# Kernel optimization log

Hardware: AMD Instinct MI355X
Metric: run time of the kernel (lower is better)

The kernel has to match this reference:

```python
import jax, jax.numpy as jnp
import numpy as np

KERNEL = 7
PAD = (KERNEL - 1) // 2


def setup_inputs() -> dict:
    key = jax.random.key(0)
    k1, k2 = jax.random.split(key)
    x = jax.random.normal(k1, (32, 256, 64, 64), dtype=jnp.float32)
    W = jax.random.normal(k2, (1, 2, KERNEL, KERNEL), dtype=jnp.float32) * 0.1
    return {"x": x, "W": W}


def reference(x, W):
    # channel-wise max and mean pooling -> [B, 2, H, W]
    x_compress = jnp.concatenate(
        [jnp.max(x, axis=1, keepdims=True), jnp.mean(x, axis=1, keepdims=True)],
        axis=1,
    )
    # 2->1 conv, same padding, no bias/bn/relu
    attn = jax.lax.conv_general_dilated(
        x_compress, W,
        window_strides=(1, 1),
        padding=[(PAD, PAD), (PAD, PAD)],
        dimension_numbers=("NCHW", "OIHW", "NCHW"),
    )
    scale = jax.nn.sigmoid(attn)  # [B, 1, H, W]
    return x * scale
```

## Files before the change

### kernel.cpp

```cpp
#include <hip/hip_runtime.h>
#include <math.h>

#define BB 32
#define CC 256
#define HH 64
#define WW 64
#define HWSZ 4096
#define CHW 1048576

typedef float f4 __attribute__((ext_vector_type(4)));

__global__ void sg_reduce(const float* __restrict__ x,
                          float* __restrict__ maxp,
                          float* __restrict__ meanp) {
    int bh = blockIdx.x;
    int b  = bh >> 6;
    int h  = bh & 63;
    int w4 = threadIdx.x & 15;
    int cg = threadIdx.x >> 4;

    const f4* base =
        reinterpret_cast<const f4*>(x + (size_t)b * CHW + h * WW) + w4;
    f4 v = base[(size_t)(cg * 16) * 1024];
    f4 mx = v, sm = v;
    #pragma unroll
    for (int cc = 1; cc < 16; ++cc) {
        f4 u = base[(size_t)(cg * 16 + cc) * 1024];
        mx.x = fmaxf(mx.x, u.x); mx.y = fmaxf(mx.y, u.y);
        mx.z = fmaxf(mx.z, u.z); mx.w = fmaxf(mx.w, u.w);
        sm += u;
    }

    __shared__ f4 lmax[16][16];
    __shared__ f4 lsum[16][16];
    lmax[cg][w4] = mx;
    lsum[cg][w4] = sm;
    __syncthreads();

    if (threadIdx.x < 16) {
        int w = threadIdx.x;
        f4 M = lmax[0][w];
        f4 S = lsum[0][w];
        #pragma unroll
        for (int g = 1; g < 16; ++g) {
            f4 m2 = lmax[g][w];
            S += lsum[g][w];
            M.x = fmaxf(M.x, m2.x); M.y = fmaxf(M.y, m2.y);
            M.z = fmaxf(M.z, m2.z); M.w = fmaxf(M.w, m2.w);
        }
        reinterpret_cast<f4*>(maxp)[bh * 16 + w] = M;
        reinterpret_cast<f4*>(meanp)[bh * 16 + w] = S * (1.0f / CC);
    }
}

__global__ void sg_conv_apply(const float* __restrict__ x,
                              const float* __restrict__ maxp,
                              const float* __restrict__ meanp,
                              const float* __restrict__ Wt,
                              float* __restrict__ out) {
    __shared__ float sscale[WW];
    int bh = blockIdx.x;
    int b  = bh >> 6;
    int h  = bh & 63;
    int tid = threadIdx.x;

    if (tid < WW) {
        int wc = tid;
        const float* mb = maxp  + b * HWSZ;
        const float* nb = meanp + b * HWSZ;
        float acc = 0.0f;
        #pragma unroll
        for (int kh = 0; kh < 7; ++kh) {
            int hh = h + kh - 3;
            if ((unsigned)hh >= (unsigned)HH) continue;
            #pragma unroll
            for (int kw = 0; kw < 7; ++kw) {
                int wcol = wc + kw - 3;
                if ((unsigned)wcol >= (unsigned)WW) continue;
                int o = (hh << 6) + wcol;
                acc = fmaf(mb[o], Wt[kh * 7 + kw],      acc);
                acc = fmaf(nb[o], Wt[49 + kh * 7 + kw], acc);
            }
        }
        sscale[wc] = 1.0f / (1.0f + __expf(-acc));
    }
    __syncthreads();

    int w4 = tid & 15;
    int cg = tid >> 4;
    f4 sc = reinterpret_cast<const f4*>(sscale)[w4];

    const f4* xb =
        reinterpret_cast<const f4*>(x + (size_t)b * CHW + h * WW) + w4;
    f4* ob =
        reinterpret_cast<f4*>(out + (size_t)b * CHW + h * WW) + w4;

    #pragma unroll
    for (int cc = 0; cc < 16; ++cc) {
        size_t off = (size_t)(cg * 16 + cc) * 1024;
        f4 v = xb[off];
        v *= sc;
        __builtin_nontemporal_store(v, ob + off);
    }
}

extern "C" void kernel_launch(void* const* d_in, const int* in_sizes, int n_in,
                              void* d_out, int out_size, void* d_ws, size_t ws_size,
                              hipStream_t stream) {
    const float* x  = (const float*)d_in[0];
    const float* Wt = (const float*)d_in[1];
    float* out = (float*)d_out;

    float* wsf   = (float*)d_ws;
    float* maxp  = wsf;
    float* meanp = wsf + BB * HWSZ;

    sg_reduce<<<BB * HH, 256, 0, stream>>>(x, maxp, meanp);
    sg_conv_apply<<<BB * HH, 256, 0, stream>>>(x, maxp, meanp, Wt, out);
}
```

Before: 73.10 us.

## Fuse reduce and conv-apply into one kernel with inter-block row flags

Merges the channel reduction and the conv/scale pass into a single kernel. Each block claims a row through an atomic ticket and keeps its 16 x-vectors per thread in registers, so x is read from HBM once instead of twice. It publishes its pooled row with a release flag and spins on flags for the neighbouring rows before computing the 7x7 conv. This adds a memset, spin-wait synchronisation and register pressure, and it relies on ticket ordering to avoid deadlock.

Result: slower. 276.7 us (+278.5%).

```diff
diff --git a/kernel.cpp b/kernel.cpp
--- a/kernel.cpp
+++ b/kernel.cpp
@@ -10,62 +10,84 @@
 
 typedef float f4 __attribute__((ext_vector_type(4)));
 
-__global__ void sg_reduce(const float* __restrict__ x,
-                          float* __restrict__ maxp,
-                          float* __restrict__ meanp) {
-    int bh = blockIdx.x;
-    int b  = bh >> 6;
-    int h  = bh & 63;
-    int w4 = threadIdx.x & 15;
-    int cg = threadIdx.x >> 4;
+__global__ void __launch_bounds__(256, 3)
+sg_fused(const float* __restrict__ x,
+         const float* __restrict__ Wt,
+         float* __restrict__ out,
+         float* __restrict__ maxp,
+         float* __restrict__ meanp,
+         int* __restrict__ flags,
+         int* __restrict__ ticket) {
+    __shared__ int s_row;
+    __shared__ float w_sh[98];
+    __shared__ alignas(16) float sscale[WW];
+    __shared__ f4 lmax[16][16];
+    __shared__ f4 lsum[16][16];
 
-    const f4* base =
+    int tid = threadIdx.x;
+    if (tid == 0) s_row = atomicAdd(ticket, 1);
+    if (tid < 98) w_sh[tid] = Wt[tid];
+    __syncthreads();
+
+    const int bh = s_row;
+    const int b  = bh >> 6;
+    const int h  = bh & 63;
+    const int w4 = tid & 15;
+    const int cg = tid >> 4;
+
+    const f4* xb =
         reinterpret_cast<const f4*>(x + (size_t)b * CHW + h * WW) + w4;
-    f4 v = base[(size_t)(cg * 16) * 1024];
-    f4 mx = v, sm = v;
+
+    f4 xr[16];
+    #pragma unroll
+    for (int cc = 0; cc < 16; ++cc)
+        xr[cc] = __builtin_nontemporal_load(xb + (size_t)(cg * 16 + cc) * 1024);
+
+    f4 mx = xr[0], sm = xr[0];
     #pragma unroll
     for (int cc = 1; cc < 16; ++cc) {
-        f4 u = base[(size_t)(cg * 16 + cc) * 1024];
+        f4 u = xr[cc];
         mx.x = fmaxf(mx.x, u.x); mx.y = fmaxf(mx.y, u.y);
         mx.z = fmaxf(mx.z, u.z); mx.w = fmaxf(mx.w, u.w);
         sm += u;
     }
-
-    __shared__ f4 lmax[16][16];
-    __shared__ f4 lsum[16][16];
     lmax[cg][w4] = mx;
     lsum[cg][w4] = sm;
     __syncthreads();
 
-    if (threadIdx.x < 16) {
-        int w = threadIdx.x;
-        f4 M = lmax[0][w];
-        f4 S = lsum[0][w];
+    if (tid < 16) {
+        f4 M = lmax[0][tid];
+        f4 S = lsum[0][tid];
         #pragma unroll
         for (int g = 1; g < 16; ++g) {
-            f4 m2 = lmax[g][w];
-            S += lsum[g][w];
+            f4 m2 = lmax[g][tid];
+            S += lsum[g][tid];
             M.x = fmaxf(M.x, m2.x); M.y = fmaxf(M.y, m2.y);
             M.z = fmaxf(M.z, m2.z); M.w = fmaxf(M.w, m2.w);
         }
-        reinterpret_cast<f4*>(maxp)[bh * 16 + w] = M;
-        reinterpret_cast<f4*>(meanp)[bh * 16 + w] = S * (1.0f / CC);
+        reinterpret_cast<f4*>(maxp)[bh * 16 + tid]  = M;
+        reinterpret_cast<f4*>(meanp)[bh * 16 + tid] = S * (1.0f / CC);
     }
-}
+    __syncthreads();
 
-__global__ void sg_conv_apply(const float* __restrict__ x,
-                              const float* __restrict__ maxp,
-                              const float* __restrict__ meanp,
-                              const float* __restrict__ Wt,
-                              float* __restrict__ out) {
-    __shared__ float sscale[WW];
-    int bh = blockIdx.x;
-    int b  = bh >> 6;
-    int h  = bh & 63;
-    int tid = threadIdx.x;
+    if (tid == 0) {
+        __threadfence();
+        __hip_atomic_store(&flags[bh], 1, __ATOMIC_RELEASE,
+                           __HIP_MEMORY_SCOPE_AGENT);
+    }
+    if (tid < 7) {
+        int hh = h - 3 + tid;
+        if (hh != h && (unsigned)hh < (unsigned)HH) {
+            const int dep = (b << 6) + hh;
+            while (__hip_atomic_load(&flags[dep], __ATOMIC_ACQUIRE,
+                                     __HIP_MEMORY_SCOPE_AGENT) == 0) {
+                __builtin_amdgcn_s_sleep(2);
+            }
+        }
+    }
+    __syncthreads();
 
     if (tid < WW) {
-        int wc = tid;
         const float* mb = maxp  + b * HWSZ;
         const float* nb = meanp + b * HWSZ;
         float acc = 0.0f;
@@ -75,32 +97,23 @@
             if ((unsigned)hh >= (unsigned)HH) continue;
             #pragma unroll
             for (int kw = 0; kw < 7; ++kw) {
-                int wcol = wc + kw - 3;
+                int wcol = tid + kw - 3;
                 if ((unsigned)wcol >= (unsigned)WW) continue;
                 int o = (hh << 6) + wcol;
-                acc = fmaf(mb[o], Wt[kh * 7 + kw],      acc);
-                acc = fmaf(nb[o], Wt[49 + kh * 7 + kw], acc);
+                acc = fmaf(mb[o], w_sh[kh * 7 + kw],      acc);
+                acc = fmaf(nb[o], w_sh[49 + kh * 7 + kw], acc);
             }
         }
-        sscale[wc] = 1.0f / (1.0f + __expf(-acc));
+        sscale[tid] = 1.0f / (1.0f + __expf(-acc));
     }
     __syncthreads();
 
-    int w4 = tid & 15;
-    int cg = tid >> 4;
     f4 sc = reinterpret_cast<const f4*>(sscale)[w4];
-
-    const f4* xb =
-        reinterpret_cast<const f4*>(x + (size_t)b * CHW + h * WW) + w4;
-    f4* ob =
-        reinterpret_cast<f4*>(out + (size_t)b * CHW + h * WW) + w4;
-
+    f4* ob = reinterpret_cast<f4*>(out + (size_t)b * CHW + h * WW) + w4;
     #pragma unroll
     for (int cc = 0; cc < 16; ++cc) {
-        size_t off = (size_t)(cg * 16 + cc) * 1024;
-        f4 v = xb[off];
-        v *= sc;
-        __builtin_nontemporal_store(v, ob + off);
+        f4 v = xr[cc] * sc;
+        __builtin_nontemporal_store(v, ob + (size_t)(cg * 16 + cc) * 1024);
     }
 }
 
@@ -114,7 +127,10 @@
     float* wsf   = (float*)d_ws;
     float* maxp  = wsf;
     float* meanp = wsf + BB * HWSZ;
+    int*   flags = (int*)(wsf + 2 * BB * HWSZ);
+    int*   ticket = flags + BB * HH;
 
-    sg_reduce<<<BB * HH, 256, 0, stream>>>(x, maxp, meanp);
-    sg_conv_apply<<<BB * HH, 256, 0, stream>>>(x, maxp, meanp, Wt, out);
+    hipMemsetAsync(flags, 0, (BB * HH + 1) * sizeof(int), stream);
+
+    sg_fused<<<BB * HH, 256, 0, stream>>>(x, Wt, out, maxp, meanp, flags, ticket);
 }
```
